# Kernel optimization log

Hardware: AMD Instinct MI355X
Metric: run time of the kernel (lower is better)

Reference implementation:

```python
import jax, jax.numpy as jnp
import numpy as np

H = 5120       # hidden_size
NH = 128       # num_heads
QLR = 1536     # q_lora_rank
DR = 64        # qk_rope_head_dim
KVLR = 512     # kv_lora_rank
DV = 128       # v_head_dim
DN = 128       # qk_nope_head_dim
DQ = 192       # q_head_dim
THETA = 10000.0
EPS = 1e-6


def _rmsnorm(x, w, eps=EPS):
    xf = x.astype(jnp.float32)
    var = jnp.mean(xf * xf, axis=-1, keepdims=True)
    return (w * (xf * jax.lax.rsqrt(var + eps))).astype(x.dtype)


def _rope(x, cos, sin):
    # Llama-style complex rotation on interleaved pairs along last dim.
    xr = x.reshape(x.shape[:-1] + (-1, 2))
    x0, x1 = xr[..., 0], xr[..., 1]
    out = jnp.stack([x0 * cos - x1 * sin, x0 * sin + x1 * cos], axis=-1)
    return out.reshape(x.shape)


def setup_inputs() -> dict:
    key = jax.random.key(0)
    ks = jax.random.split(key, 8)
    b, kv_len = 2, 2048
    s = 0.02  # scaled-down normal init for numerical sanity (math unchanged)
    return {
        "hidden_states": jax.random.normal(ks[0], (b, 1, H), jnp.float32),
        "compressed_kv_normed_cache": jax.random.normal(ks[1], (b, kv_len, KVLR), jnp.float32),
        "k_pe_cache": jax.random.normal(ks[2], (b, kv_len, DR), jnp.float32),
        "q_a_w": jax.random.normal(ks[3], (QLR, H), jnp.float32) * s,
        "q_a_ln_w": jnp.ones((QLR,), jnp.float32),
        "q_b_w": jax.random.normal(ks[4], (NH * DQ, QLR), jnp.float32) * s,
        "kv_b_w": jax.random.normal(ks[5], (NH * (DN + DV), KVLR), jnp.float32) * s,
        "o_w": jax.random.normal(ks[6], (H, NH * DV), jnp.float32) * s,
    }


def reference(hidden_states, compressed_kv_normed_cache, k_pe_cache,
              q_a_w, q_a_ln_w, q_b_w, kv_b_w, o_w):
    b = hidden_states.shape[0]
    kv_len = k_pe_cache.shape[1]

    # Q path: down-proj -> RMSNorm -> up-proj
    q_a = jnp.einsum('bqh,rh->bqr', hidden_states, q_a_w)          # [b,1,QLR]
    q_a = _rmsnorm(q_a, q_a_ln_w)
    q = jnp.einsum('bqr,or->bqo', q_a, q_b_w).reshape(b, NH, DQ)   # q_len==1
    q_nope, q_pe = q[..., :DN], q[..., DN:]                        # [b,NH,128],[b,NH,64]

    # RoPE tables
    inv_freq = 1.0 / (THETA ** (jnp.arange(0, DR, 2, dtype=jnp.float32) / DR))  # [32]
    ang = jnp.arange(kv_len, dtype=jnp.float32)[:, None] * inv_freq             # [kv_len,32]
    cos, sin = jnp.cos(ang), jnp.sin(ang)

    # query rotated at position kv_len-1 (torch code repeats q then takes last slot)
    q_pe = _rope(q_pe, cos[-1], sin[-1])                           # [b,NH,64]
    k_pe = _rope(k_pe_cache, cos[None], sin[None])                 # [b,kv_len,64]

    # KV decompression (shared latent -> per-head nope-key and value)
    kv = jnp.einsum('bkc,oc->bko', compressed_kv_normed_cache, kv_b_w)
    kv = kv.reshape(b, kv_len, NH, DN + DV)
    k_nope, v = kv[..., :DN], kv[..., DN:]                         # [b,kv,NH,128] each

    # scores: nope part + rope part (k_pe broadcast across heads)
    scores = (jnp.einsum('bhd,bkhd->bhk', q_nope, k_nope)
              + jnp.einsum('bhd,bkd->bhk', q_pe, k_pe)) * (DQ ** -0.5)
    attn = jax.nn.softmax(scores.astype(jnp.float32), axis=-1).astype(hidden_states.dtype)

    out = jnp.einsum('bhk,bkhd->bhd', attn, v).reshape(b, 1, NH * DV)
    return jnp.einsum('bqo,ho->bqh', out, o_w)                     # [b,1,H]
```

## Files before the change

### kernel.cpp

```cpp
#include <hip/hip_runtime.h>
#include <math.h>

constexpr int kH    = 5120;
constexpr int kQLR  = 1536;
constexpr int kNH   = 128;
constexpr int kDQ   = 192;
constexpr int kDN   = 128;
constexpr int kDR   = 64;
constexpr int kKVLR = 512;
constexpr int kDV   = 128;

template<int IN>
__global__ __launch_bounds__(256) void gemv2b_k(const float* __restrict__ W,
                                                const float* __restrict__ x,
                                                float* __restrict__ y, int R) {
  int lane = threadIdx.x & 63, wave = threadIdx.x >> 6;
  int row = blockIdx.x * 4 + wave;
  constexpr int F4 = IN / 256;
  const float4* W4 = (const float4*)(W + (size_t)row * IN);
  const float4* x0 = (const float4*)x;
  const float4* x1 = (const float4*)(x + IN);
  float a0 = 0.f, a1 = 0.f;
#pragma unroll 4
  for (int i = 0; i < F4; ++i) {
    int idx = lane + (i << 6);
    float4 w = W4[idx];
    float4 u = x0[idx];
    float4 v = x1[idx];
    a0 = fmaf(w.x, u.x, fmaf(w.y, u.y, fmaf(w.z, u.z, fmaf(w.w, u.w, a0))));
    a1 = fmaf(w.x, v.x, fmaf(w.y, v.y, fmaf(w.z, v.z, fmaf(w.w, v.w, a1))));
  }
#pragma unroll
  for (int off = 32; off > 0; off >>= 1) {
    a0 += __shfl_down(a0, off, 64);
    a1 += __shfl_down(a1, off, 64);
  }
  if (lane == 0) {
    y[row] = a0;
    y[(size_t)R + row] = a1;
  }
}

__global__ __launch_bounds__(256) void rmsnorm_k(const float* __restrict__ qa,
                                                 const float* __restrict__ w,
                                                 float* __restrict__ out) {
  int b = blockIdx.x, t = threadIdx.x;
  const float* x = qa + (size_t)b * kQLR;
  float s = 0.f;
  for (int i = t; i < kQLR; i += 256) { float v = x[i]; s = fmaf(v, v, s); }
  __shared__ float red[4];
#pragma unroll
  for (int off = 32; off > 0; off >>= 1) s += __shfl_down(s, off, 64);
  if ((t & 63) == 0) red[t >> 6] = s;
  __syncthreads();
  float tot = red[0] + red[1] + red[2] + red[3];
  float scale = rsqrtf(tot / (float)kQLR + 1e-6f);
  for (int i = t; i < kQLR; i += 256) out[(size_t)b * kQLR + i] = x[i] * scale * w[i];
}

__global__ __launch_bounds__(256) void rope_q_k(float* __restrict__ q, int pos) {
  int p = blockIdx.x * 256 + threadIdx.x;
  int i = p & 31;
  int h = (p >> 5) & (kNH - 1);
  int b = p >> 12;
  float inv = powf(10000.0f, -(float)i * (1.0f / 32.0f));
  float ang = (float)pos * inv;
  float s, c;
  sincosf(ang, &s, &c);
  float* base = q + ((size_t)b * kNH + h) * kDQ + kDN + 2 * i;
  float x0 = base[0], x1 = base[1];
  base[0] = x0 * c - x1 * s;
  base[1] = x0 * s + x1 * c;
}

__global__ __launch_bounds__(256) void rope_k_k(const float* __restrict__ kin,
                                                float* __restrict__ kout, int KV) {
  int p = blockIdx.x * 256 + threadIdx.x;
  int i = p & 31;
  int bk = p >> 5;
  int b = bk / KV;
  int k = bk - b * KV;
  float inv = powf(10000.0f, -(float)i * (1.0f / 32.0f));
  float ang = (float)k * inv;
  float s, c;
  sincosf(ang, &s, &c);
  const float* src = kin + ((size_t)b * KV + k) * kDR + 2 * i;
  float* dst = kout + ((size_t)b * KV + k) * kDR + 2 * i;
  float x0 = src[0], x1 = src[1];
  dst[0] = x0 * c - x1 * s;
  dst[1] = x0 * s + x1 * c;
}

__global__ __launch_bounds__(128) void qabs_k(const float* __restrict__ q,
                                              const float* __restrict__ kvw,
                                              float* __restrict__ qabs) {
  int h = blockIdx.x, half = blockIdx.y;
  int t = threadIdx.x;
  __shared__ float qn[2 * kDN];
  qn[t]        = q[(size_t)h * kDQ + t];
  qn[128 + t]  = q[((size_t)kNH + h) * kDQ + t];
  __syncthreads();
  int col = half * 256 + t * 2;
  float a0x = 0.f, a0y = 0.f, a1x = 0.f, a1y = 0.f;
  const float* wb = kvw + (size_t)h * 256 * kKVLR + col;
#pragma unroll 4
  for (int d = 0; d < kDN; ++d) {
    float2 w = *(const float2*)(wb + (size_t)d * kKVLR);
    float q0 = qn[d], q1 = qn[128 + d];
    a0x = fmaf(q0, w.x, a0x); a0y = fmaf(q0, w.y, a0y);
    a1x = fmaf(q1, w.x, a1x); a1y = fmaf(q1, w.y, a1y);
  }
  *(float2*)(qabs + (size_t)h * kKVLR + col)           = make_float2(a0x, a0y);
  *(float2*)(qabs + ((size_t)kNH + h) * kKVLR + col)   = make_float2(a1x, a1y);
}

__global__ __launch_bounds__(256) void scores_k(const float* __restrict__ qabs,
                                                const float* __restrict__ qfull,
                                                const float* __restrict__ c,
                                                const float* __restrict__ kper,
                                                float* __restrict__ scores, int KV) {
  int kc = blockIdx.x, hg = blockIdx.y, b = blockIdx.z;
  int t = threadIdx.x, lane = t & 63, wave = t >> 6;
  int h0 = __builtin_amdgcn_readfirstlane(hg * 32 + wave * 8);
  int k0 = kc * 64;
  __shared__ float cl[64 * 129];
  __shared__ float kl[64 * 65];
  float acc[8];
#pragma unroll
  for (int j = 0; j < 8; ++j) acc[j] = 0.f;

  {
    const float4* src = (const float4*)(kper + ((size_t)b * KV + k0) * kDR);
#pragma unroll
    for (int i = 0; i < 4; ++i) {
      int idx = t + i * 256;
      int r = idx >> 4, c4 = idx & 15;
      float4 v = src[r * 16 + c4];
      float* d = &kl[r * 65 + (c4 << 2)];
      d[0] = v.x; d[1] = v.y; d[2] = v.z; d[3] = v.w;
    }
  }

  for (int cch = 0; cch < 4; ++cch) {
    __syncthreads();
    const float* cb = c + ((size_t)b * KV + k0) * kKVLR + cch * 128;
#pragma unroll
    for (int i = 0; i < 8; ++i) {
      int idx = t + i * 256;
      int r = idx >> 5, c4 = idx & 31;
      float4 v = *(const float4*)(cb + (size_t)r * kKVLR + (c4 << 2));
      float* d = &cl[r * 129 + (c4 << 2)];
      d[0] = v.x; d[1] = v.y; d[2] = v.z; d[3] = v.w;
    }
    __syncthreads();
    const float* qb = qabs + ((size_t)b * kNH + h0) * kKVLR + cch * 128;
#pragma unroll 4
    for (int cc = 0; cc < 128; ++cc) {
      float cv = cl[lane * 129 + cc];
#pragma unroll
      for (int j = 0; j < 8; ++j)
        acc[j] = fmaf(cv, qb[(size_t)j * kKVLR + cc], acc[j]);
    }
  }

  {
    const float* qp = qfull + ((size_t)b * kNH + h0) * kDQ + kDN;
#pragma unroll 4
    for (int i = 0; i < 64; ++i) {
      float kv = kl[lane * 65 + i];
#pragma unroll
      for (int j = 0; j < 8; ++j)
        acc[j] = fmaf(kv, qp[j * kDQ + i], acc[j]);
    }
  }

  const float scale = 1.0f / sqrtf(192.0f);
#pragma unroll
  for (int j = 0; j < 8; ++j)
    scores[((size_t)b * kNH + h0 + j) * KV + k0 + lane] = acc[j] * scale;
}

__global__ __launch_bounds__(256) void softmax_k(float* __restrict__ sc, int KV) {
  int t = threadIdx.x;
  float* row = sc + (size_t)blockIdx.x * KV;
  float vals[8];
  float m = -1e30f;
#pragma unroll
  for (int i = 0; i < 8; ++i) {
    vals[i] = row[t + i * 256];
    m = fmaxf(m, vals[i]);
  }
  __shared__ float red[4];
#pragma unroll
  for (int off = 32; off > 0; off >>= 1) m = fmaxf(m, __shfl_down(m, off, 64));
  if ((t & 63) == 0) red[t >> 6] = m;
  __syncthreads();
  m = fmaxf(fmaxf(red[0], red[1]), fmaxf(red[2], red[3]));
  __syncthreads();
  float s = 0.f;
#pragma unroll
  for (int i = 0; i < 8; ++i) {
    vals[i] = __expf(vals[i] - m);
    s += vals[i];
  }
#pragma unroll
  for (int off = 32; off > 0; off >>= 1) s += __shfl_down(s, off, 64);
  if ((t & 63) == 0) red[t >> 6] = s;
  __syncthreads();
  s = red[0] + red[1] + red[2] + red[3];
  float inv = 1.0f / s;
#pragma unroll
  for (int i = 0; i < 8; ++i) row[t + i * 256] = vals[i] * inv;
}

__global__ __launch_bounds__(256) void ctx_partial_k(const float* __restrict__ attn,
                                                     const float* __restrict__ c,
                                                     float* __restrict__ ctxp, int KV) {
  int ks = blockIdx.x, hg = blockIdx.y, b = blockIdx.z;
  int t = threadIdx.x;
  int klen = KV >> 4;
  int k0 = ks * klen;
  float2 acc[16];
#pragma unroll
  for (int j = 0; j < 16; ++j) acc[j] = make_float2(0.f, 0.f);
  const float2* c2 = (const float2*)(c + (size_t)b * KV * kKVLR) + t;
  const float* arow = attn + ((size_t)b * kNH + hg * 16) * KV + k0;
  for (int k = 0; k < klen; ++k) {
    float2 cv = c2[(size_t)(k0 + k) * (kKVLR / 2)];
#pragma unroll
    for (int j = 0; j < 16; ++j) {
      float a = arow[(size_t)j * KV + k];
      acc[j].x = fmaf(a, cv.x, acc[j].x);
      acc[j].y = fmaf(a, cv.y, acc[j].y);
    }
  }
#pragma unroll
  for (int j = 0; j < 16; ++j) {
    float2* dst = (float2*)(ctxp + (((size_t)ks * 2 + b) * kNH + hg * 16 + j) * kKVLR);
    dst[t] = acc[j];
  }
}

__global__ __launch_bounds__(256) void vproj_k(const float* __restrict__ ctxp,
                                               const float* __restrict__ kvw,
                                               float* __restrict__ oh) {
  int h = blockIdx.x, half = blockIdx.y;
  int t = threadIdx.x, lane = t & 63, wave = t >> 6;
  __shared__ float cl[2 * kKVLR];
  {
    int b = t >> 7, c4 = t & 127;
    float4 s = make_float4(0.f, 0.f, 0.f, 0.f);
#pragma unroll
    for (int ks = 0; ks < 16; ++ks) {
      const float4* p = (const float4*)(ctxp + (((size_t)ks * 2 + b) * kNH + h) * kKVLR);
      float4 v = p[c4];
      s.x += v.x; s.y += v.y; s.z += v.z; s.w += v.w;
    }
    *(float4*)&cl[b * kKVLR + (c4 << 2)] = s;
  }
  __syncthreads();
  float cr0[8], cr1[8];
#pragma unroll
  for (int j = 0; j < 8; ++j) {
    cr0[j] = cl[lane * 8 + j];
    cr1[j] = cl[kKVLR + lane * 8 + j];
  }
  for (int i = 0; i < 16; ++i) {
    int d = half * 64 + wave * 16 + i;
    const float4* w4 = (const float4*)(kvw + ((size_t)h * 256 + 128 + d) * kKVLR + lane * 8);
    float4 wa = w4[0], wb = w4[1];
    float s0 = wa.x * cr0[0] + wa.y * cr0[1] + wa.z * cr0[2] + wa.w * cr0[3]
             + wb.x * cr0[4] + wb.y * cr0[5] + wb.z * cr0[6] + wb.w * cr0[7];
    float s1 = wa.x * cr1[0] + wa.y * cr1[1] + wa.z * cr1[2] + wa.w * cr1[3]
             + wb.x * cr1[4] + wb.y * cr1[5] + wb.z * cr1[6] + wb.w * cr1[7];
#pragma unroll
    for (int off = 32; off > 0; off >>= 1) {
      s0 += __shfl_down(s0, off, 64);
      s1 += __shfl_down(s1, off, 64);
    }
    if (lane == 0) {
      oh[(size_t)h * kDV + d] = s0;
      oh[((size_t)kNH + h) * kDV + d] = s1;
    }
  }
}

extern "C" void kernel_launch(void* const* d_in, const int* in_sizes, int n_in,
                              void* d_out, int out_size, void* d_ws, size_t ws_size,
                              hipStream_t stream) {
  const float* hs   = (const float*)d_in[0];
  const float* ckv  = (const float*)d_in[1];
  const float* kpe  = (const float*)d_in[2];
  const float* qaw  = (const float*)d_in[3];
  const float* qlnw = (const float*)d_in[4];
  const float* qbw  = (const float*)d_in[5];
  const float* kvbw = (const float*)d_in[6];
  const float* ow   = (const float*)d_in[7];
  float* out = (float*)d_out;

  int B  = in_sizes[0] / kH;
  int KV = in_sizes[2] / (B * kDR);

  float* ws   = (float*)d_ws;
  float* qa   = ws;
  float* qan  = qa + 4096;
  float* q    = qan + 4096;
  float* qabs = q + (size_t)B * kNH * kDQ;
  float* kper = qabs + (size_t)B * kNH * kKVLR;
  float* sc   = kper + (size_t)B * KV * kDR;
  float* ctxp = sc + (size_t)B * kNH * KV;
  float* oh   = ctxp + (size_t)16 * B * kNH * kKVLR;

  gemv2b_k<kH><<<kQLR / 4, 256, 0, stream>>>(qaw, hs, qa, kQLR);
  rmsnorm_k<<<B, 256, 0, stream>>>(qa, qlnw, qan);
  gemv2b_k<kQLR><<<(kNH * kDQ) / 4, 256, 0, stream>>>(qbw, qan, q, kNH * kDQ);
  rope_q_k<<<(B * kNH * 32) / 256, 256, 0, stream>>>(q, KV - 1);
  rope_k_k<<<(B * KV * 32) / 256, 256, 0, stream>>>(kpe, kper, KV);
  qabs_k<<<dim3(kNH, 2), 128, 0, stream>>>(q, kvbw, qabs);
  scores_k<<<dim3(KV / 64, 4, B), 256, 0, stream>>>(qabs, q, ckv, kper, sc, KV);
  softmax_k<<<B * kNH, 256, 0, stream>>>(sc, KV);
  ctx_partial_k<<<dim3(16, 8, B), 256, 0, stream>>>(sc, ckv, ctxp, KV);
  vproj_k<<<dim3(kNH, 2), 256, 0, stream>>>(ctxp, kvbw, oh);
  gemv2b_k<kNH * kDV><<<kH / 4, 256, 0, stream>>>(ow, oh, out, kH);
}
```

Baseline: 732.5 us.

## Split GEMVs and attention kernels across more blocks with atomic reductions

Reworks most kernels to expose more parallelism. The GEMVs now compute two rows per wave and split the input dimension four ways, combining partial sums with atomics into memset buffers. qabs splits the head dimension into four chunks, also reduced with atomics. Scores uses half as many heads per wave, and ctx_partial stages the attention weights in shared memory over more, shorter k-chunks. vproj is split into quarters, which leaves fewer idle CUs on the memory-bound passes, at the cost of extra memsets, atomics and nondeterministic float summation order.

```diff
diff --git a/kernel.cpp b/kernel.cpp
--- a/kernel.cpp
+++ b/kernel.cpp
@@ -10,34 +10,51 @@
 constexpr int kKVLR = 512;
 constexpr int kDV   = 128;
 
-template<int IN>
-__global__ __launch_bounds__(256) void gemv2b_k(const float* __restrict__ W,
-                                                const float* __restrict__ x,
-                                                float* __restrict__ y, int R) {
+template<int IN, int SPLIT, bool ATOMIC>
+__global__ __launch_bounds__(256) void gemv2_k(const float* __restrict__ W,
+                                               const float* __restrict__ x,
+                                               float* __restrict__ y, int R) {
+  constexpr int CH = IN / SPLIT;
+  constexpr int F4 = CH / 256;
   int lane = threadIdx.x & 63, wave = threadIdx.x >> 6;
-  int row = blockIdx.x * 4 + wave;
-  constexpr int F4 = IN / 256;
-  const float4* W4 = (const float4*)(W + (size_t)row * IN);
-  const float4* x0 = (const float4*)x;
-  const float4* x1 = (const float4*)(x + IN);
-  float a0 = 0.f, a1 = 0.f;
+  int r0 = blockIdx.x * 8 + wave * 2;
+  int c0 = blockIdx.y * CH;
+  const float4* W0 = (const float4*)(W + (size_t)r0 * IN + c0);
+  const float4* W1 = (const float4*)(W + (size_t)(r0 + 1) * IN + c0);
+  const float4* x0 = (const float4*)(x + c0);
+  const float4* x1 = (const float4*)(x + IN + c0);
+  float a00 = 0.f, a01 = 0.f, a10 = 0.f, a11 = 0.f;
 #pragma unroll 4
   for (int i = 0; i < F4; ++i) {
     int idx = lane + (i << 6);
-    float4 w = W4[idx];
+    float4 w0 = W0[idx];
+    float4 w1 = W1[idx];
     float4 u = x0[idx];
     float4 v = x1[idx];
-    a0 = fmaf(w.x, u.x, fmaf(w.y, u.y, fmaf(w.z, u.z, fmaf(w.w, u.w, a0))));
-    a1 = fmaf(w.x, v.x, fmaf(w.y, v.y, fmaf(w.z, v.z, fmaf(w.w, v.w, a1))));
+    a00 = fmaf(w0.x,u.x,fmaf(w0.y,u.y,fmaf(w0.z,u.z,fmaf(w0.w,u.w,a00))));
+    a01 = fmaf(w0.x,v.x,fmaf(w0.y,v.y,fmaf(w0.z,v.z,fmaf(w0.w,v.w,a01))));
+    a10 = fmaf(w1.x,u.x,fmaf(w1.y,u.y,fmaf(w1.z,u.z,fmaf(w1.w,u.w,a10))));
+    a11 = fmaf(w1.x,v.x,fmaf(w1.y,v.y,fmaf(w1.z,v.z,fmaf(w1.w,v.w,a11))));
   }
 #pragma unroll
   for (int off = 32; off > 0; off >>= 1) {
-    a0 += __shfl_down(a0, off, 64);
-    a1 += __shfl_down(a1, off, 64);
+    a00 += __shfl_down(a00, off, 64);
+    a01 += __shfl_down(a01, off, 64);
+    a10 += __shfl_down(a10, off, 64);
+    a11 += __shfl_down(a11, off, 64);
   }
   if (lane == 0) {
-    y[row] = a0;
-    y[(size_t)R + row] = a1;
+    if (ATOMIC) {
+      atomicAdd(&y[r0], a00);
+      atomicAdd(&y[(size_t)R + r0], a01);
+      atomicAdd(&y[r0 + 1], a10);
+      atomicAdd(&y[(size_t)R + r0 + 1], a11);
+    } else {
+      y[r0] = a00;
+      y[(size_t)R + r0] = a01;
+      y[r0 + 1] = a10;
+      y[(size_t)R + r0 + 1] = a11;
+    }
   }
 }
 
@@ -91,27 +108,30 @@
   dst[1] = x0 * s + x1 * c;
 }
 
-__global__ __launch_bounds__(128) void qabs_k(const float* __restrict__ q,
+__global__ __launch_bounds__(256) void qabs_k(const float* __restrict__ q,
                                               const float* __restrict__ kvw,
                                               float* __restrict__ qabs) {
-  int h = blockIdx.x, half = blockIdx.y;
+  int h = blockIdx.x, ds = blockIdx.y;
   int t = threadIdx.x;
-  __shared__ float qn[2 * kDN];
-  qn[t]        = q[(size_t)h * kDQ + t];
-  qn[128 + t]  = q[((size_t)kNH + h) * kDQ + t];
-  __syncthreads();
-  int col = half * 256 + t * 2;
+  __shared__ float qn[2][32];
+  if (t < 64) {
+    int b = t >> 5, d = t & 31;
+    qn[b][d] = q[((size_t)b * kNH + h) * kDQ + ds * 32 + d];
+  }
+  __syncthreads();
   float a0x = 0.f, a0y = 0.f, a1x = 0.f, a1y = 0.f;
-  const float* wb = kvw + (size_t)h * 256 * kKVLR + col;
+  const float* wb = kvw + ((size_t)h * 256 + ds * 32) * kKVLR + t * 2;
 #pragma unroll 4
-  for (int d = 0; d < kDN; ++d) {
+  for (int d = 0; d < 32; ++d) {
     float2 w = *(const float2*)(wb + (size_t)d * kKVLR);
-    float q0 = qn[d], q1 = qn[128 + d];
+    float q0 = qn[0][d], q1 = qn[1][d];
     a0x = fmaf(q0, w.x, a0x); a0y = fmaf(q0, w.y, a0y);
     a1x = fmaf(q1, w.x, a1x); a1y = fmaf(q1, w.y, a1y);
   }
-  *(float2*)(qabs + (size_t)h * kKVLR + col)           = make_float2(a0x, a0y);
-  *(float2*)(qabs + ((size_t)kNH + h) * kKVLR + col)   = make_float2(a1x, a1y);
+  float* p0 = qabs + (size_t)h * kKVLR + t * 2;
+  float* p1 = qabs + ((size_t)kNH + h) * kKVLR + t * 2;
+  atomicAdd(p0, a0x); atomicAdd(p0 + 1, a0y);
+  atomicAdd(p1, a1x); atomicAdd(p1 + 1, a1y);
 }
 
 __global__ __launch_bounds__(256) void scores_k(const float* __restrict__ qabs,
@@ -121,13 +141,11 @@
                                                 float* __restrict__ scores, int KV) {
   int kc = blockIdx.x, hg = blockIdx.y, b = blockIdx.z;
   int t = threadIdx.x, lane = t & 63, wave = t >> 6;
-  int h0 = __builtin_amdgcn_readfirstlane(hg * 32 + wave * 8);
+  int h0 = __builtin_amdgcn_readfirstlane(hg * 16 + wave * 4);
   int k0 = kc * 64;
   __shared__ float cl[64 * 129];
   __shared__ float kl[64 * 65];
-  float acc[8];
-#pragma unroll
-  for (int j = 0; j < 8; ++j) acc[j] = 0.f;
+  float acc[4] = {0.f, 0.f, 0.f, 0.f};
 
   {
     const float4* src = (const float4*)(kper + ((size_t)b * KV + k0) * kDR);
@@ -158,7 +176,7 @@
     for (int cc = 0; cc < 128; ++cc) {
       float cv = cl[lane * 129 + cc];
 #pragma unroll
-      for (int j = 0; j < 8; ++j)
+      for (int j = 0; j < 4; ++j)
         acc[j] = fmaf(cv, qb[(size_t)j * kKVLR + cc], acc[j]);
     }
   }
@@ -169,14 +187,14 @@
     for (int i = 0; i < 64; ++i) {
       float kv = kl[lane * 65 + i];
 #pragma unroll
-      for (int j = 0; j < 8; ++j)
+      for (int j = 0; j < 4; ++j)
         acc[j] = fmaf(kv, qp[j * kDQ + i], acc[j]);
     }
   }
 
   const float scale = 1.0f / sqrtf(192.0f);
 #pragma unroll
-  for (int j = 0; j < 8; ++j)
+  for (int j = 0; j < 4; ++j)
     scores[((size_t)b * kNH + h0 + j) * KV + k0 + lane] = acc[j] * scale;
 }
 
@@ -218,25 +236,38 @@
                                                      float* __restrict__ ctxp, int KV) {
   int ks = blockIdx.x, hg = blockIdx.y, b = blockIdx.z;
   int t = threadIdx.x;
-  int klen = KV >> 4;
-  int k0 = ks * klen;
+  int k0 = ks * 64, h0 = hg * 16;
+  __shared__ float al[64 * 20];
+#pragma unroll
+  for (int i = 0; i < 4; ++i) {
+    int idx = t + i * 256;
+    int j = idx >> 6, k = idx & 63;
+    al[k * 20 + j] = attn[((size_t)b * kNH + h0 + j) * KV + k0 + k];
+  }
+  __syncthreads();
   float2 acc[16];
 #pragma unroll
   for (int j = 0; j < 16; ++j) acc[j] = make_float2(0.f, 0.f);
-  const float2* c2 = (const float2*)(c + (size_t)b * KV * kKVLR) + t;
-  const float* arow = attn + ((size_t)b * kNH + hg * 16) * KV + k0;
-  for (int k = 0; k < klen; ++k) {
-    float2 cv = c2[(size_t)(k0 + k) * (kKVLR / 2)];
-#pragma unroll
-    for (int j = 0; j < 16; ++j) {
-      float a = arow[(size_t)j * KV + k];
-      acc[j].x = fmaf(a, cv.x, acc[j].x);
-      acc[j].y = fmaf(a, cv.y, acc[j].y);
+  const float2* c2 = (const float2*)(c + ((size_t)b * KV + k0) * kKVLR);
+#pragma unroll 2
+  for (int k = 0; k < 64; ++k) {
+    float2 cv = c2[k * (kKVLR / 2) + t];
+#pragma unroll
+    for (int j4 = 0; j4 < 4; ++j4) {
+      float4 av = *(const float4*)&al[k * 20 + j4 * 4];
+      acc[j4*4+0].x = fmaf(av.x, cv.x, acc[j4*4+0].x);
+      acc[j4*4+0].y = fmaf(av.x, cv.y, acc[j4*4+0].y);
+      acc[j4*4+1].x = fmaf(av.y, cv.x, acc[j4*4+1].x);
+      acc[j4*4+1].y = fmaf(av.y, cv.y, acc[j4*4+1].y);
+      acc[j4*4+2].x = fmaf(av.z, cv.x, acc[j4*4+2].x);
+      acc[j4*4+2].y = fmaf(av.z, cv.y, acc[j4*4+2].y);
+      acc[j4*4+3].x = fmaf(av.w, cv.x, acc[j4*4+3].x);
+      acc[j4*4+3].y = fmaf(av.w, cv.y, acc[j4*4+3].y);
     }
   }
 #pragma unroll
   for (int j = 0; j < 16; ++j) {
-    float2* dst = (float2*)(ctxp + (((size_t)ks * 2 + b) * kNH + hg * 16 + j) * kKVLR);
+    float2* dst = (float2*)(ctxp + (((size_t)ks * 2 + b) * kNH + h0 + j) * kKVLR);
     dst[t] = acc[j];
   }
 }
@@ -244,30 +275,31 @@
 __global__ __launch_bounds__(256) void vproj_k(const float* __restrict__ ctxp,
                                                const float* __restrict__ kvw,
                                                float* __restrict__ oh) {
-  int h = blockIdx.x, half = blockIdx.y;
+  int h = blockIdx.x, dq = blockIdx.y;
   int t = threadIdx.x, lane = t & 63, wave = t >> 6;
-  __shared__ float cl[2 * kKVLR];
+  __shared__ float cf[2 * kKVLR];
   {
-    int b = t >> 7, c4 = t & 127;
+    int b = t >> 7, g = t & 127;
     float4 s = make_float4(0.f, 0.f, 0.f, 0.f);
-#pragma unroll
-    for (int ks = 0; ks < 16; ++ks) {
+#pragma unroll 8
+    for (int ks = 0; ks < 32; ++ks) {
       const float4* p = (const float4*)(ctxp + (((size_t)ks * 2 + b) * kNH + h) * kKVLR);
-      float4 v = p[c4];
+      float4 v = p[g];
       s.x += v.x; s.y += v.y; s.z += v.z; s.w += v.w;
     }
-    *(float4*)&cl[b * kKVLR + (c4 << 2)] = s;
+    *(float4*)&cf[b * kKVLR + (g << 2)] = s;
   }
   __syncthreads();
   float cr0[8], cr1[8];
 #pragma unroll
   for (int j = 0; j < 8; ++j) {
-    cr0[j] = cl[lane * 8 + j];
-    cr1[j] = cl[kKVLR + lane * 8 + j];
-  }
-  for (int i = 0; i < 16; ++i) {
-    int d = half * 64 + wave * 16 + i;
-    const float4* w4 = (const float4*)(kvw + ((size_t)h * 256 + 128 + d) * kKVLR + lane * 8);
+    cr0[j] = cf[lane * 8 + j];
+    cr1[j] = cf[kKVLR + lane * 8 + j];
+  }
+#pragma unroll
+  for (int i = 0; i < 8; ++i) {
+    int d = dq * 32 + wave * 8 + i;
+    const float4* w4 = (const float4*)(kvw + ((size_t)h * 256 + 128 + d) * kKVLR) + lane * 2;
     float4 wa = w4[0], wb = w4[1];
     float s0 = wa.x * cr0[0] + wa.y * cr0[1] + wa.z * cr0[2] + wa.w * cr0[3]
              + wb.x * cr0[4] + wb.y * cr0[5] + wb.z * cr0[6] + wb.w * cr0[7];
@@ -309,17 +341,21 @@
   float* kper = qabs + (size_t)B * kNH * kKVLR;
   float* sc   = kper + (size_t)B * KV * kDR;
   float* ctxp = sc + (size_t)B * kNH * KV;
-  float* oh   = ctxp + (size_t)16 * B * kNH * kKVLR;
-
-  gemv2b_k<kH><<<kQLR / 4, 256, 0, stream>>>(qaw, hs, qa, kQLR);
+  float* oh   = ctxp + (size_t)32 * B * kNH * kKVLR;
+
+  hipMemsetAsync(qa, 0, (size_t)B * kQLR * sizeof(float), stream);
+  hipMemsetAsync(qabs, 0, (size_t)B * kNH * kKVLR * sizeof(float), stream);
+  hipMemsetAsync(out, 0, (size_t)out_size * sizeof(float), stream);
+
+  gemv2_k<kH, 4, true><<<dim3(kQLR / 8, 4), 256, 0, stream>>>(qaw, hs, qa, kQLR);
   rmsnorm_k<<<B, 256, 0, stream>>>(qa, qlnw, qan);
-  gemv2b_k<kQLR><<<(kNH * kDQ) / 4, 256, 0, stream>>>(qbw, qan, q, kNH * kDQ);
+  gemv2_k<kQLR, 1, false><<<dim3((kNH * kDQ) / 8, 1), 256, 0, stream>>>(qbw, qan, q, kNH * kDQ);
   rope_q_k<<<(B * kNH * 32) / 256, 256, 0, stream>>>(q, KV - 1);
   rope_k_k<<<(B * KV * 32) / 256, 256, 0, stream>>>(kpe, kper, KV);
-  qabs_k<<<dim3(kNH, 2), 128, 0, stream>>>(q, kvbw, qabs);
-  scores_k<<<dim3(KV / 64, 4, B), 256, 0, stream>>>(qabs, q, ckv, kper, sc, KV);
+  qabs_k<<<dim3(kNH, 4), 256, 0, stream>>>(q, kvbw, qabs);
+  scores_k<<<dim3(KV / 64, 8, B), 256, 0, stream>>>(qabs, q, ckv, kper, sc, KV);
   softmax_k<<<B * kNH, 256, 0, stream>>>(sc, KV);
-  ctx_partial_k<<<dim3(16, 8, B), 256, 0, stream>>>(sc, ckv, ctxp, KV);
-  vproj_k<<<dim3(kNH, 2), 256, 0, stream>>>(ctxp, kvbw, oh);
-  gemv2b_k<kNH * kDV><<<kH / 4, 256, 0, stream>>>(ow, oh, out, kH);
-}
+  ctx_partial_k<<<dim3(32, 8, B), 256, 0, stream>>>(sc, ckv, ctxp, KV);
+  vproj_k<<<dim3(kNH, 4), 256, 0, stream>>>(ctxp, kvbw, oh);
+  gemv2_k<kNH * kDV, 4, true><<<dim3(kH / 8, 4), 256, 0, stream>>>(ow, oh, out, kH);
+}
```

Result: faster. 668.1 us (-8.8%).
